# Optimization experiments

Hardware: AMD Instinct MI355X
Metric: run time of the kernel (lower is better)

Reference implementation:

```python
import jax, jax.numpy as jnp
import numpy as np

N = 50000   # total nodes
E = 600000  # total edges
F = 128     # in_features == hidden_features
H = 128
L = 4       # layers_count
B = 256     # number of graphs in batch
M = 200     # molecule_features
OUT = 12    # out_features
MH = H // 4 # molecular head width


def setup_inputs() -> dict:
    key = jax.random.key(0)
    ks = jax.random.split(key, 16)
    x = jax.random.normal(ks[0], (N, F), dtype=jnp.float32)
    edge_index = jax.random.randint(ks[1], (2, E), 0, N, dtype=jnp.int64)
    # sorted segment ids; guarantee every graph has >=1 node
    batch = jnp.sort(jnp.concatenate([
        jnp.arange(B, dtype=jnp.int64),
        jax.random.randint(ks[2], (N - B,), 0, B, dtype=jnp.int64)]))
    molecule_features = jax.random.normal(ks[3], (B, M), dtype=jnp.float32)
    s = 0.05
    Ws = jax.random.normal(ks[4], (L, H, H), dtype=jnp.float32) * s
    bs = jnp.zeros((L, H), dtype=jnp.float32)
    Wm = jax.random.normal(ks[5], (M, MH), dtype=jnp.float32) * s
    bm = jnp.zeros((MH,), dtype=jnp.float32)
    gamma = jnp.ones((MH,), dtype=jnp.float32)   # BatchNorm1d affine (eval mode, running stats 0/1)
    beta = jnp.zeros((MH,), dtype=jnp.float32)
    W1 = jax.random.normal(ks[6], (2 * H + MH, H), dtype=jnp.float32) * s  # mlp in = 288
    b1 = jnp.zeros((H,), dtype=jnp.float32)
    W2 = jax.random.normal(ks[7], (H, OUT), dtype=jnp.float32) * s
    b2 = jnp.zeros((OUT,), dtype=jnp.float32)
    return dict(x=x, edge_index=edge_index, batch=batch,
                molecule_features=molecule_features, Ws=Ws, bs=bs,
                Wm=Wm, bm=bm, gamma=gamma, beta=beta,
                W1=W1, b1=b1, W2=W2, b2=b2)


def gcn_conv(x, src, dst, W, b):
    # GCNConv: D^{-1/2} (A + I) D^{-1/2} X W + b, degrees include self loops
    ones = jnp.ones((E,), dtype=x.dtype)
    deg = jax.ops.segment_sum(ones, dst, num_segments=N) + 1.0  # self loop
    dis = jax.lax.rsqrt(deg)
    norm = dis[src] * dis[dst]                      # [E]
    xw = x @ W                                      # [N,H]
    msg = xw[src] * norm[:, None]                   # gather + scale
    agg = jax.ops.segment_sum(msg, dst, num_segments=N)
    agg = agg + xw * (dis * dis)[:, None]           # self-loop term
    return agg + b


def reference(x, edge_index, batch, molecule_features, Ws, bs, Wm, bm,
              gamma, beta, W1, b1, W2, b2):
    src, dst = edge_index[0], edge_index[1]
    h = x
    for l in range(L):
        y = jax.nn.relu(gcn_conv(h, src, dst, Ws[l], bs[l]))
        h = y + h  # residual (in == hidden); dropout is identity in eval
    max_pool = jax.ops.segment_max(h, batch, num_segments=B)
    add_pool = jax.ops.segment_sum(h, batch, num_segments=B)
    # molecular head: Linear -> Dropout(eval=identity) -> BatchNorm1d(eval) -> ReLU
    mol = molecule_features @ Wm + bm
    mol = jax.nn.relu(mol * gamma + beta)  # running_mean=0, running_var=1
    z = jnp.concatenate((max_pool, add_pool, mol), axis=1)  # [B, 288]
    z = jax.nn.relu(z @ W1 + b1)
    return z @ W2 + b2  # [B, OUT]
```

## Files before the change

### kernel.cpp

```cpp
#include <hip/hip_runtime.h>
#include <hip/hip_fp16.h>
#include <math.h>

static constexpr int NN  = 50000;
static constexpr int NE  = 600000;
static constexpr int HD  = 128;
static constexpr int NL  = 4;
static constexpr int NB  = 256;
static constexpr int NM  = 200;
static constexpr int NO  = 12;
static constexpr int NMH = 32;
static constexpr int CST = 64;

#define MAX4(ac, b) { (ac).x = fmaxf((ac).x,(b).x); (ac).y = fmaxf((ac).y,(b).y); (ac).z = fmaxf((ac).z,(b).z); (ac).w = fmaxf((ac).w,(b).w); }
#define ADD4(ac, b) { (ac).x += (b).x; (ac).y += (b).y; (ac).z += (b).z; (ac).w += (b).w; }

typedef short bfx8 __attribute__((ext_vector_type(8)));
typedef float f32x4 __attribute__((ext_vector_type(4)));

__device__ __forceinline__ unsigned short f2bf(float f) {
  unsigned int u = __float_as_uint(f);
  unsigned int r = (u + 0x7fffu + ((u >> 16) & 1u)) >> 16;
  return (unsigned short)r;
}
__device__ __forceinline__ float bflo(unsigned int p) { return __uint_as_float(p << 16); }
__device__ __forceinline__ float bfhi(unsigned int p) { return __uint_as_float(p & 0xffff0000u); }
__device__ __forceinline__ float h2f_hi(unsigned e) {
  return __half2float(__ushort_as_half((unsigned short)(e >> 16)));
}

__global__ void k_hist(const int* __restrict__ dst, int* __restrict__ counts) {
  int e = blockIdx.x * blockDim.x + threadIdx.x;
  if (e < NE) atomicAdd(&counts[dst[e]], 1);
}

static constexpr int NT_TOBF = NN * HD / 4;
static constexpr int NT_WT   = NL * HD * HD;
static constexpr int NT_GOFF = NT_TOBF + NT_WT;
static constexpr int NT_DIS  = NT_GOFF + NN;
static constexpr int NT_ALL  = NT_DIS + NN;

__global__ void k_setup(const float4* __restrict__ x4, ushort4* __restrict__ xbf4,
                        const float* __restrict__ Ws, unsigned short* __restrict__ wT,
                        const int* __restrict__ batch, int* __restrict__ goffs,
                        const int* __restrict__ counts, float* __restrict__ dis) {
  int i = blockIdx.x * blockDim.x + threadIdx.x;
  if (i < NT_TOBF) {
    float4 v = x4[i];
    xbf4[i] = make_ushort4(f2bf(v.x), f2bf(v.y), f2bf(v.z), f2bf(v.w));
  } else if (i < NT_GOFF) {
    int j = i - NT_TOBF;
    int l = j >> 14, rem = j & 16383, n = rem >> 7, k = rem & 127;
    wT[j] = f2bf(Ws[l * 16384 + k * 128 + n]);
  } else if (i < NT_DIS) {
    int j = i - NT_GOFF;
    int b = batch[j];
    if (j == 0) {
      for (int g = 0; g <= b; ++g) goffs[g] = 0;
    } else {
      int pb = batch[j - 1];
      for (int g = pb + 1; g <= b; ++g) goffs[g] = j;
    }
    if (j == NN - 1) goffs[NB] = NN;
  } else if (i < NT_ALL) {
    int j = i - NT_DIS;
    dis[j] = rsqrtf((float)(counts[j] + 1));
  }
}

__global__ void k_fill(const int* __restrict__ src, const int* __restrict__ dst,
                       const float* __restrict__ dis, int* __restrict__ cur,
                       unsigned* __restrict__ csr) {
  int e = blockIdx.x * blockDim.x + threadIdx.x;
  if (e < NE) {
    int d = dst[e];
    int s = src[e];
    int p = atomicAdd(&cur[d], 1);
    unsigned hb = (unsigned)__half_as_ushort(__float2half(dis[s]));
    csr[d * CST + p] = (hb << 16) | (unsigned)s;
  }
}

__launch_bounds__(256)
__global__ void k_gemm_mfma(const unsigned short* __restrict__ A,
                            const unsigned short* __restrict__ WT,
                            unsigned short* __restrict__ C) {
  const int wave = threadIdx.x >> 6;
  const int lane = threadIdx.x & 63;
  const int m_base = blockIdx.x * 128 + wave * 32;
  const int lr = lane & 15;
  const int kg = lane >> 4;

  f32x4 acc[2][8];
#pragma unroll
  for (int mi = 0; mi < 2; ++mi)
#pragma unroll
    for (int nj = 0; nj < 8; ++nj) acc[mi][nj] = (f32x4){0.f, 0.f, 0.f, 0.f};

  int ra0 = m_base + lr;       if (ra0 > NN - 1) ra0 = NN - 1;
  int ra1 = m_base + 16 + lr;  if (ra1 > NN - 1) ra1 = NN - 1;

#pragma unroll
  for (int kb = 0; kb < 4; ++kb) {
    const int k0 = kb * 32 + kg * 8;
    bfx8 a0 = *(const bfx8*)&A[(size_t)ra0 * HD + k0];
    bfx8 a1 = *(const bfx8*)&A[(size_t)ra1 * HD + k0];
#pragma unroll
    for (int nj = 0; nj < 8; ++nj) {
      bfx8 b = *(const bfx8*)&WT[(nj * 16 + lr) * HD + k0];
      acc[0][nj] = __builtin_amdgcn_mfma_f32_16x16x32_bf16(a0, b, acc[0][nj], 0, 0, 0);
      acc[1][nj] = __builtin_amdgcn_mfma_f32_16x16x32_bf16(a1, b, acc[1][nj], 0, 0, 0);
    }
  }

  const int col = lane & 15;
  const int rbase = (lane >> 4) * 4;
#pragma unroll
  for (int mi = 0; mi < 2; ++mi) {
#pragma unroll
    for (int r = 0; r < 4; ++r) {
      int row = m_base + mi * 16 + rbase + r;
      if (row < NN) {
#pragma unroll
        for (int nj = 0; nj < 8; ++nj) {
          C[(size_t)row * HD + nj * 16 + col] = f2bf(acc[mi][nj][r]);
        }
      }
    }
  }
}

#define AGGE(e, p) { float nm = h2f_hi(e) * dn; \
    acc[0] += nm * bflo((p).x); acc[1] += nm * bfhi((p).x); \
    acc[2] += nm * bflo((p).y); acc[3] += nm * bfhi((p).y); \
    acc[4] += nm * bflo((p).z); acc[5] += nm * bfhi((p).z); \
    acc[6] += nm * bflo((p).w); acc[7] += nm * bfhi((p).w); }

__launch_bounds__(256)
__global__ void k_agg16(const unsigned short* __restrict__ xw, const float* __restrict__ dis,
                        const int* __restrict__ deg, const unsigned* __restrict__ csr,
                        const float* __restrict__ bias, const unsigned short* __restrict__ hinb,
                        unsigned short* __restrict__ houtb) {
  int slot = threadIdx.x >> 4;
  int lane = threadIdx.x & 15;
  int n = blockIdx.x * 16 + slot;
  if (n >= NN) return;

  const uint4* xw4 = (const uint4*)xw;

  float dn = dis[n];
  float acc[8];
  {
    uint4 p = xw4[(size_t)n * 16 + lane];
    float sl = dn * dn;
    acc[0] = bflo(p.x) * sl; acc[1] = bfhi(p.x) * sl;
    acc[2] = bflo(p.y) * sl; acc[3] = bfhi(p.y) * sl;
    acc[4] = bflo(p.z) * sl; acc[5] = bfhi(p.z) * sl;
    acc[6] = bflo(p.w) * sl; acc[7] = bfhi(p.w) * sl;
  }

  int s0 = n * CST;
  int s1 = s0 + deg[n];
  int idx = s0;
  for (; idx + 8 <= s1; idx += 8) {
    unsigned e0 = csr[idx],     e1 = csr[idx + 1], e2 = csr[idx + 2], e3 = csr[idx + 3];
    unsigned e4 = csr[idx + 4], e5 = csr[idx + 5], e6 = csr[idx + 6], e7 = csr[idx + 7];
    uint4 p0 = xw4[(size_t)(e0 & 0xffffu) * 16 + lane];
    uint4 p1 = xw4[(size_t)(e1 & 0xffffu) * 16 + lane];
    uint4 p2 = xw4[(size_t)(e2 & 0xffffu) * 16 + lane];
    uint4 p3 = xw4[(size_t)(e3 & 0xffffu) * 16 + lane];
    uint4 p4 = xw4[(size_t)(e4 & 0xffffu) * 16 + lane];
    uint4 p5 = xw4[(size_t)(e5 & 0xffffu) * 16 + lane];
    uint4 p6 = xw4[(size_t)(e6 & 0xffffu) * 16 + lane];
    uint4 p7 = xw4[(size_t)(e7 & 0xffffu) * 16 + lane];
    AGGE(e0, p0); AGGE(e1, p1); AGGE(e2, p2); AGGE(e3, p3);
    AGGE(e4, p4); AGGE(e5, p5); AGGE(e6, p6); AGGE(e7, p7);
  }
  for (; idx + 4 <= s1; idx += 4) {
    unsigned e0 = csr[idx], e1 = csr[idx + 1], e2 = csr[idx + 2], e3 = csr[idx + 3];
    uint4 p0 = xw4[(size_t)(e0 & 0xffffu) * 16 + lane];
    uint4 p1 = xw4[(size_t)(e1 & 0xffffu) * 16 + lane];
    uint4 p2 = xw4[(size_t)(e2 & 0xffffu) * 16 + lane];
    uint4 p3 = xw4[(size_t)(e3 & 0xffffu) * 16 + lane];
    AGGE(e0, p0); AGGE(e1, p1); AGGE(e2, p2); AGGE(e3, p3);
  }
  for (; idx < s1; ++idx) {
    unsigned e0 = csr[idx];
    uint4 p0 = xw4[(size_t)(e0 & 0xffffu) * 16 + lane];
    AGGE(e0, p0);
  }

  float4 ba = *(const float4*)&bias[lane * 8];
  float4 bb = *(const float4*)&bias[lane * 8 + 4];
  uint4 hp = ((const uint4*)hinb)[(size_t)n * 16 + lane];
  float o0 = fmaxf(acc[0] + ba.x, 0.f) + bflo(hp.x);
  float o1 = fmaxf(acc[1] + ba.y, 0.f) + bfhi(hp.x);
  float o2 = fmaxf(acc[2] + ba.z, 0.f) + bflo(hp.y);
  float o3 = fmaxf(acc[3] + ba.w, 0.f) + bfhi(hp.y);
  float o4 = fmaxf(acc[4] + bb.x, 0.f) + bflo(hp.z);
  float o5 = fmaxf(acc[5] + bb.y, 0.f) + bfhi(hp.z);
  float o6 = fmaxf(acc[6] + bb.z, 0.f) + bflo(hp.w);
  float o7 = fmaxf(acc[7] + bb.w, 0.f) + bfhi(hp.w);
  uint4 ov;
  ov.x = (unsigned)f2bf(o0) | ((unsigned)f2bf(o1) << 16);
  ov.y = (unsigned)f2bf(o2) | ((unsigned)f2bf(o3) << 16);
  ov.z = (unsigned)f2bf(o4) | ((unsigned)f2bf(o5) << 16);
  ov.w = (unsigned)f2bf(o6) | ((unsigned)f2bf(o7) << 16);
  ((uint4*)houtb)[(size_t)n * 16 + lane] = ov;
}

__launch_bounds__(1024)
__global__ void k_pool(const unsigned short* __restrict__ hb, const int* __restrict__ goffs,
                       float* __restrict__ pooled) {
  __shared__ float4 smax[32][32];
  __shared__ float4 ssum[32][32];
  int g = blockIdx.x;
  int slot = threadIdx.x >> 5;
  int lane = threadIdx.x & 31;
  int a = goffs[g], bnd = goffs[g + 1];
  const uint2* hb2 = (const uint2*)hb;

  float4 mx = make_float4(-INFINITY, -INFINITY, -INFINITY, -INFINITY);
  float4 sm = make_float4(0.f, 0.f, 0.f, 0.f);
  for (int i = a + slot; i < bnd; i += 32) {
    uint2 p = hb2[(size_t)i * 32 + lane];
    float4 v = make_float4(bflo(p.x), bfhi(p.x), bflo(p.y), bfhi(p.y));
    MAX4(mx, v);
    ADD4(sm, v);
  }
  smax[slot][lane] = mx;
  ssum[slot][lane] = sm;
  __syncthreads();
#pragma unroll
  for (int off = 16; off >= 1; off >>= 1) {
    if (slot < off) {
      float4 m2 = smax[slot + off][lane];
      float4 s2 = ssum[slot + off][lane];
      float4 m1 = smax[slot][lane];
      float4 s1 = ssum[slot][lane];
      MAX4(m1, m2);
      ADD4(s1, s2);
      smax[slot][lane] = m1;
      ssum[slot][lane] = s1;
    }
    __syncthreads();
  }
  if (slot == 0) {
    *(float4*)&pooled[g * 256 + lane * 4]       = smax[0][lane];
    *(float4*)&pooled[g * 256 + 128 + lane * 4] = ssum[0][lane];
  }
}

__global__ void k_head(const float* __restrict__ pooled, const float* __restrict__ mf,
                       const float* __restrict__ Wm, const float* __restrict__ bm,
                       const float* __restrict__ gamma, const float* __restrict__ beta,
                       const float* __restrict__ W1, const float* __restrict__ b1,
                       const float* __restrict__ W2, const float* __restrict__ b2,
                       float* __restrict__ out) {
  __shared__ float z[288];
  __shared__ float z1[128];
  int g = blockIdx.x, t = threadIdx.x;
  z[t] = pooled[g * 256 + t];
  z[128 + t] = pooled[g * 256 + 128 + t];
  if (t < NMH) {
    float acc = bm[t];
    for (int k = 0; k < NM; ++k) acc += mf[g * NM + k] * Wm[k * NMH + t];
    acc = acc * gamma[t] + beta[t];
    z[256 + t] = fmaxf(acc, 0.f);
  }
  __syncthreads();
  float acc = b1[t];
  for (int k = 0; k < 288; ++k) acc += z[k] * W1[k * HD + t];
  z1[t] = fmaxf(acc, 0.f);
  __syncthreads();
  if (t < NO) {
    float a2 = b2[t];
    for (int k = 0; k < HD; ++k) a2 += z1[k] * W2[k * NO + t];
    out[g * NO + t] = a2;
  }
}

extern "C" void kernel_launch(void* const* d_in, const int* in_sizes, int n_in,
                              void* d_out, int out_size, void* d_ws, size_t ws_size,
                              hipStream_t stream) {
  const float* x     = (const float*)d_in[0];
  const int*   eidx  = (const int*)d_in[1];
  const int*   batch = (const int*)d_in[2];
  const float* mf    = (const float*)d_in[3];
  const float* Ws    = (const float*)d_in[4];
  const float* bs    = (const float*)d_in[5];
  const float* Wm    = (const float*)d_in[6];
  const float* bm    = (const float*)d_in[7];
  const float* gamma = (const float*)d_in[8];
  const float* beta  = (const float*)d_in[9];
  const float* W1    = (const float*)d_in[10];
  const float* b1    = (const float*)d_in[11];
  const float* W2    = (const float*)d_in[12];
  const float* b2    = (const float*)d_in[13];
  float* out = (float*)d_out;

  const int* src = eidx;
  const int* dst = eidx + NE;

  char* w = (char*)d_ws;
  size_t off = 0;
  auto alloc = [&](size_t bytes) -> void* {
    void* p = w + off;
    off += (bytes + 255) & ~(size_t)255;
    return p;
  };
  float* dis    = (float*)alloc((size_t)NN * 4);
  unsigned short* xw  = (unsigned short*)alloc((size_t)NN * HD * 2);
  unsigned short* xbf = (unsigned short*)alloc((size_t)NN * HD * 2);
  unsigned short* hbf = (unsigned short*)alloc((size_t)NN * HD * 2);
  unsigned short* wT  = (unsigned short*)alloc((size_t)NL * HD * HD * 2);
  int* counts   = (int*)alloc((size_t)NN * 4);
  int* cur      = (int*)alloc((size_t)NN * 4);
  unsigned* csr = (unsigned*)alloc((size_t)NN * CST * 4);
  int* goffs    = (int*)alloc((size_t)(NB + 1) * 4);
  float* pooled = (float*)alloc((size_t)NB * 256 * 4);
  (void)ws_size;

  size_t zspan = (size_t)((char*)(cur + NN) - (char*)counts);
  hipMemsetAsync(counts, 0, zspan, stream);

  k_hist<<<(NE + 255) / 256, 256, 0, stream>>>(dst, counts);
  k_setup<<<(NT_ALL + 255) / 256, 256, 0, stream>>>((const float4*)x, (ushort4*)xbf,
                                                    Ws, wT, batch, goffs, counts, dis);
  k_fill<<<(NE + 255) / 256, 256, 0, stream>>>(src, dst, dis, cur, csr);

  for (int l = 0; l < NL; ++l) {
    const unsigned short* gin_bf = (l == 0) ? xbf : hbf;
    k_gemm_mfma<<<(NN + 127) / 128, 256, 0, stream>>>(gin_bf, wT + (size_t)l * HD * HD, xw);
    k_agg16<<<(NN + 15) / 16, 256, 0, stream>>>(xw, dis, counts, csr, bs + (size_t)l * HD, gin_bf, hbf);
  }

  k_pool<<<NB, 1024, 0, stream>>>(hbf, goffs, pooled);
  k_head<<<NB, 128, 0, stream>>>(pooled, mf, Wm, bm, gamma, beta, W1, b1, W2, b2, out);
}
```

Baseline: 274.8 us.

## Sort nodes by degree for balanced aggregation and fuse pooling with head

Nodes are bucketed by in-degree using a histogram, a single-thread scan and an atomic scatter into a permutation. The aggregation kernel then processes nodes in degree order, so nodes sharing a wavefront have similar edge-loop trip counts and divergence drops. The degree histogram kernel now reads four edges per thread, and the pooling and MLP head kernels are merged into one launch, removing the pooled intermediate buffer. The permutation makes output writes and self-row reads non-contiguous and adds a tiny serial scan kernel.

```diff
diff --git a/kernel.cpp b/kernel.cpp
--- a/kernel.cpp
+++ b/kernel.cpp
@@ -29,9 +29,15 @@
   return __half2float(__ushort_as_half((unsigned short)(e >> 16)));
 }
 
-__global__ void k_hist(const int* __restrict__ dst, int* __restrict__ counts) {
-  int e = blockIdx.x * blockDim.x + threadIdx.x;
-  if (e < NE) atomicAdd(&counts[dst[e]], 1);
+__global__ void k_hist(const int4* __restrict__ dst4, int* __restrict__ counts) {
+  int i = blockIdx.x * blockDim.x + threadIdx.x;
+  if (i < NE / 4) {
+    int4 d = dst4[i];
+    atomicAdd(&counts[d.x], 1);
+    atomicAdd(&counts[d.y], 1);
+    atomicAdd(&counts[d.z], 1);
+    atomicAdd(&counts[d.w], 1);
+  }
 }
 
 static constexpr int NT_TOBF = NN * HD / 4;
@@ -43,7 +49,8 @@
 __global__ void k_setup(const float4* __restrict__ x4, ushort4* __restrict__ xbf4,
                         const float* __restrict__ Ws, unsigned short* __restrict__ wT,
                         const int* __restrict__ batch, int* __restrict__ goffs,
-                        const int* __restrict__ counts, float* __restrict__ dis) {
+                        const int* __restrict__ counts, float* __restrict__ dis,
+                        int* __restrict__ bins) {
   int i = blockIdx.x * blockDim.x + threadIdx.x;
   if (i < NT_TOBF) {
     float4 v = x4[i];
@@ -64,13 +71,23 @@
     if (j == NN - 1) goffs[NB] = NN;
   } else if (i < NT_ALL) {
     int j = i - NT_DIS;
-    dis[j] = rsqrtf((float)(counts[j] + 1));
+    int d = counts[j];
+    dis[j] = rsqrtf((float)(d + 1));
+    atomicAdd(&bins[d > CST ? CST : d], 1);
+  }
+}
+
+__global__ void k_bscan(int* __restrict__ bins) {
+  if (threadIdx.x == 0) {
+    int run = 0;
+    for (int d = 0; d <= CST; ++d) { int c = bins[d]; bins[d] = run; run += c; }
   }
 }
 
 __global__ void k_fill(const int* __restrict__ src, const int* __restrict__ dst,
                        const float* __restrict__ dis, int* __restrict__ cur,
-                       unsigned* __restrict__ csr) {
+                       unsigned* __restrict__ csr, const int* __restrict__ counts,
+                       int* __restrict__ bins, int* __restrict__ perm) {
   int e = blockIdx.x * blockDim.x + threadIdx.x;
   if (e < NE) {
     int d = dst[e];
@@ -78,6 +95,11 @@
     int p = atomicAdd(&cur[d], 1);
     unsigned hb = (unsigned)__half_as_ushort(__float2half(dis[s]));
     csr[d * CST + p] = (hb << 16) | (unsigned)s;
+  } else if (e < NE + NN) {
+    int n = e - NE;
+    int d = counts[n]; if (d > CST) d = CST;
+    int p = atomicAdd(&bins[d], 1);
+    perm[p] = n;
   }
 }
 
@@ -140,11 +162,12 @@
 __global__ void k_agg16(const unsigned short* __restrict__ xw, const float* __restrict__ dis,
                         const int* __restrict__ deg, const unsigned* __restrict__ csr,
                         const float* __restrict__ bias, const unsigned short* __restrict__ hinb,
-                        unsigned short* __restrict__ houtb) {
+                        unsigned short* __restrict__ houtb, const int* __restrict__ perm) {
   int slot = threadIdx.x >> 4;
   int lane = threadIdx.x & 15;
-  int n = blockIdx.x * 16 + slot;
-  if (n >= NN) return;
+  int i = blockIdx.x * 16 + slot;
+  if (i >= NN) return;
+  int n = perm[i];
 
   const uint4* xw4 = (const uint4*)xw;
 
@@ -210,10 +233,17 @@
 }
 
 __launch_bounds__(1024)
-__global__ void k_pool(const unsigned short* __restrict__ hb, const int* __restrict__ goffs,
-                       float* __restrict__ pooled) {
+__global__ void k_poolhead(const unsigned short* __restrict__ hb, const int* __restrict__ goffs,
+                           const float* __restrict__ mf,
+                           const float* __restrict__ Wm, const float* __restrict__ bm,
+                           const float* __restrict__ gamma, const float* __restrict__ beta,
+                           const float* __restrict__ W1, const float* __restrict__ b1,
+                           const float* __restrict__ W2, const float* __restrict__ b2,
+                           float* __restrict__ out) {
   __shared__ float4 smax[32][32];
   __shared__ float4 ssum[32][32];
+  __shared__ float z[288];
+  __shared__ float z1[128];
   int g = blockIdx.x;
   int slot = threadIdx.x >> 5;
   int lane = threadIdx.x & 31;
@@ -246,34 +276,26 @@
     __syncthreads();
   }
   if (slot == 0) {
-    *(float4*)&pooled[g * 256 + lane * 4]       = smax[0][lane];
-    *(float4*)&pooled[g * 256 + 128 + lane * 4] = ssum[0][lane];
-  }
-}
-
-__global__ void k_head(const float* __restrict__ pooled, const float* __restrict__ mf,
-                       const float* __restrict__ Wm, const float* __restrict__ bm,
-                       const float* __restrict__ gamma, const float* __restrict__ beta,
-                       const float* __restrict__ W1, const float* __restrict__ b1,
-                       const float* __restrict__ W2, const float* __restrict__ b2,
-                       float* __restrict__ out) {
-  __shared__ float z[288];
-  __shared__ float z1[128];
-  int g = blockIdx.x, t = threadIdx.x;
-  z[t] = pooled[g * 256 + t];
-  z[128 + t] = pooled[g * 256 + 128 + t];
-  if (t < NMH) {
+    *(float4*)&z[lane * 4]       = smax[0][lane];
+    *(float4*)&z[128 + lane * 4] = ssum[0][lane];
+  }
+  if (threadIdx.x < NMH) {
+    int t = threadIdx.x;
     float acc = bm[t];
     for (int k = 0; k < NM; ++k) acc += mf[g * NM + k] * Wm[k * NMH + t];
     acc = acc * gamma[t] + beta[t];
     z[256 + t] = fmaxf(acc, 0.f);
   }
   __syncthreads();
-  float acc = b1[t];
-  for (int k = 0; k < 288; ++k) acc += z[k] * W1[k * HD + t];
-  z1[t] = fmaxf(acc, 0.f);
+  if (threadIdx.x < 128) {
+    int t = threadIdx.x;
+    float acc = b1[t];
+    for (int k = 0; k < 288; ++k) acc += z[k] * W1[k * HD + t];
+    z1[t] = fmaxf(acc, 0.f);
+  }
   __syncthreads();
-  if (t < NO) {
+  if (threadIdx.x < NO) {
+    int t = threadIdx.x;
     float a2 = b2[t];
     for (int k = 0; k < HD; ++k) a2 += z1[k] * W2[k * NO + t];
     out[g * NO + t] = a2;
@@ -316,25 +338,27 @@
   unsigned short* wT  = (unsigned short*)alloc((size_t)NL * HD * HD * 2);
   int* counts   = (int*)alloc((size_t)NN * 4);
   int* cur      = (int*)alloc((size_t)NN * 4);
+  int* bins     = (int*)alloc(128 * 4);
   unsigned* csr = (unsigned*)alloc((size_t)NN * CST * 4);
+  int* perm     = (int*)alloc((size_t)NN * 4);
   int* goffs    = (int*)alloc((size_t)(NB + 1) * 4);
-  float* pooled = (float*)alloc((size_t)NB * 256 * 4);
   (void)ws_size;
 
-  size_t zspan = (size_t)((char*)(cur + NN) - (char*)counts);
+  size_t zspan = (size_t)((char*)(bins + 128) - (char*)counts);
   hipMemsetAsync(counts, 0, zspan, stream);
 
-  k_hist<<<(NE + 255) / 256, 256, 0, stream>>>(dst, counts);
+  k_hist<<<(NE / 4 + 255) / 256, 256, 0, stream>>>((const int4*)dst, counts);
   k_setup<<<(NT_ALL + 255) / 256, 256, 0, stream>>>((const float4*)x, (ushort4*)xbf,
-                                                    Ws, wT, batch, goffs, counts, dis);
-  k_fill<<<(NE + 255) / 256, 256, 0, stream>>>(src, dst, dis, cur, csr);
+                                                    Ws, wT, batch, goffs, counts, dis, bins);
+  k_bscan<<<1, 64, 0, stream>>>(bins);
+  k_fill<<<(NE + NN + 255) / 256, 256, 0, stream>>>(src, dst, dis, cur, csr, counts, bins, perm);
 
   for (int l = 0; l < NL; ++l) {
     const unsigned short* gin_bf = (l == 0) ? xbf : hbf;
     k_gemm_mfma<<<(NN + 127) / 128, 256, 0, stream>>>(gin_bf, wT + (size_t)l * HD * HD, xw);
-    k_agg16<<<(NN + 15) / 16, 256, 0, stream>>>(xw, dis, counts, csr, bs + (size_t)l * HD, gin_bf, hbf);
-  }
-
-  k_pool<<<NB, 1024, 0, stream>>>(hbf, goffs, pooled);
-  k_head<<<NB, 128, 0, stream>>>(pooled, mf, Wm, bm, gamma, beta, W1, b1, W2, b2, out);
-}
+    k_agg16<<<(NN + 15) / 16, 256, 0, stream>>>(xw, dis, counts, csr, bs + (size_t)l * HD,
+                                                gin_bf, hbf, perm);
+  }
+
+  k_poolhead<<<NB, 1024, 0, stream>>>(hbf, goffs, mf, Wm, bm, gamma, beta, W1, b1, W2, b2, out);
+}
```

Result: slower. 572.8 us (+108.5%).
